# Kernel optimization log

Measured on AMD Instinct MI355X. Metric: run time of the kernel, lower is better.

## Reference

```python
import jax, jax.numpy as jnp
import numpy as np

V, D, H, L, E = 50000, 512, 512, 4, 40000


def setup_inputs() -> dict:
    key = jax.random.key(0)
    k1, k2, k3 = jax.random.split(key, 3)
    node_embeddings = jax.random.normal(k1, (V, D), dtype=jnp.float32)
    adjacency = jax.random.randint(k2, (L, E, 2), 0, V, dtype=jnp.int32)
    W = jax.random.normal(k3, (L, D, H), dtype=jnp.float32) * (1.0 / np.sqrt(D))
    return {"node_embeddings": node_embeddings, "adjacency": adjacency, "W": W}


def reference(node_embeddings, adjacency, W):
    # adjacency: [L, E, 2] with [:, :, 0] = source node, [:, :, 1] = target node
    src = adjacency[..., 0]  # [L, E]
    tgt = adjacency[..., 1]  # [L, E]
    # Gather source states per edge and apply per-edge-type linear message fn.
    # edge_source_states: [L, E, D]; messages: [L, E, H]
    messages = jnp.einsum("led,ldh->leh", node_embeddings[src], W)
    # Scatter-aggregate (sum) all messages to their target nodes.
    num_nodes = node_embeddings.shape[0]
    aggregated = jax.ops.segment_sum(
        messages.reshape(-1, messages.shape[-1]),  # [L*E, H]
        tgt.reshape(-1),
        num_segments=num_nodes,
    )  # [V, H]
    # message_activation_before_aggregation = False -> activation after aggregation
    return jax.nn.relu(aggregated)
```

## Files before the change

### kernel.cpp

```cpp
#include <hip/hip_runtime.h>
#include <hip/hip_bf16.h>

#define NV 50000
#define VP2 50176
#define ND 512
#define NH 512
#define NL 4
#define NE 40000
#define CAP 16
#define KTOT 2048
#define NKT 32
#define NWG2 392

typedef short bf16x8 __attribute__((ext_vector_type(8)));
typedef float f32x4  __attribute__((ext_vector_type(4)));

__device__ __forceinline__ unsigned short f2bf(float f) {
    unsigned int u = __float_as_uint(f);
    u += 0x7FFFu + ((u >> 16) & 1u);
    return (unsigned short)(u >> 16);
}
__device__ __forceinline__ unsigned pack_bf2(float x, float y) {
    return (unsigned)f2bf(x) | ((unsigned)f2bf(y) << 16);
}

#define GLL16(gp, lp) __builtin_amdgcn_global_load_lds( \
    (const __attribute__((address_space(1))) void*)(gp), \
    (__attribute__((address_space(3))) void*)(lp), 16, 0, 0)

#define SBAR   __builtin_amdgcn_s_barrier()
#define SCHED0 __builtin_amdgcn_sched_barrier(0)
#define PRIO1  __builtin_amdgcn_s_setprio(1)
#define PRIO0  __builtin_amdgcn_s_setprio(0)
#define VMCNT0 asm volatile("s_waitcnt vmcnt(0)" ::: "memory")
#define LGKM0  asm volatile("s_waitcnt lgkmcnt(0)" ::: "memory")

__global__ void wt2_kernel(const float* __restrict__ W, unsigned short* __restrict__ Wt2) {
    int idx = blockIdx.x * 256 + threadIdx.x;
    int l = idx >> 18;
    int r = idx & 262143;
    int k = r >> 9;
    int h = r & 511;
    Wt2[((size_t)h << 11) + (l << 9) + k] = f2bf(W[idx]);
}

__global__ void place_kernel(const int* __restrict__ adj, int* __restrict__ cnt,
                             int* __restrict__ list) {
    int i = blockIdx.x * 256 + threadIdx.x;
    int2 p = ((const int2*)adj)[i];
    int l = i / NE;
    int cell = p.y * NL + l;
    int pos = atomicAdd(&cnt[cell], 1);
    if (pos < CAP) list[cell * CAP + pos] = p.x;
}

__global__ void __launch_bounds__(256)
agg_pull(const float* __restrict__ emb, const int* __restrict__ cnt,
         const int* __restrict__ list, unsigned* __restrict__ agg2) {
    const int wid  = blockIdx.x * 4 + (threadIdx.x >> 6);
    const int lane = threadIdx.x & 63;
    const int t    = wid >> 2;
    const int l    = wid & 3;
    const int cell = wid;
    const size_t dst = (size_t)t * 1024 + l * 256 + lane;

    int n = cnt[cell]; if (n > CAP) n = CAP;
    const int* lst = list + cell * CAP;

    float2 s0 = {0.f,0.f}, s1 = {0.f,0.f}, s2 = {0.f,0.f}, s3 = {0.f,0.f};
    int j = 0;
    for (; j + 2 <= n; j += 2) {
        const float2* p0 = (const float2*)(emb + (size_t)lst[j]     * ND) + lane;
        const float2* p1 = (const float2*)(emb + (size_t)lst[j + 1] * ND) + lane;
        float2 a0 = p0[0], a1 = p0[64], a2 = p0[128], a3 = p0[192];
        float2 b0 = p1[0], b1 = p1[64], b2 = p1[128], b3 = p1[192];
        s0.x += a0.x + b0.x; s0.y += a0.y + b0.y;
        s1.x += a1.x + b1.x; s1.y += a1.y + b1.y;
        s2.x += a2.x + b2.x; s2.y += a2.y + b2.y;
        s3.x += a3.x + b3.x; s3.y += a3.y + b3.y;
    }
    if (j < n) {
        const float2* p0 = (const float2*)(emb + (size_t)lst[j] * ND) + lane;
        float2 a0 = p0[0], a1 = p0[64], a2 = p0[128], a3 = p0[192];
        s0.x += a0.x; s0.y += a0.y;  s1.x += a1.x; s1.y += a1.y;
        s2.x += a2.x; s2.y += a2.y;  s3.x += a3.x; s3.y += a3.y;
    }
    agg2[dst]       = pack_bf2(s0.x, s0.y);
    agg2[dst + 64]  = pack_bf2(s1.x, s1.y);
    agg2[dst + 128] = pack_bf2(s2.x, s2.y);
    agg2[dst + 192] = pack_bf2(s3.x, s3.y);
}

__device__ __forceinline__ void stage_ht(
    int s, int t0, int n0, int wave, int lane,
    const unsigned short* __restrict__ agg2, const unsigned short* __restrict__ Wt2,
    unsigned short* sa0, unsigned short* sa1,
    unsigned short* sb0, unsigned short* sb1) {
    const int tile  = s >> 2, part = s & 3;
    const int lr8   = (part & 1) << 7;
    const int rowin = lane >> 3;
    const int slt   = (lane & 7) ^ rowin;
    const bool isA  = part < 2;
    const unsigned short* gsrc = isA ? agg2 : Wt2;
    const int gr0 = isA ? t0 : n0;
    unsigned short* ldsbase = isA ? ((tile & 1) ? sa1 : sa0)
                                  : ((tile & 1) ? sb1 : sb0);
#pragma unroll
    for (int c = 0; c < 2; ++c) {
        const int lr = lr8 + (wave * 2 + c) * 8;
        const unsigned short* src = gsrc
            + (size_t)(gr0 + lr + rowin) * KTOT + tile * 64 + slt * 8;
        GLL16(src, ldsbase + lr * 64);
    }
}

template<bool STG, bool VMW>
__device__ __forceinline__ void group4(
    int kt, int t0, int n0, int wave, int lane, int wm, int wn,
    const unsigned short* __restrict__ agg2, const unsigned short* __restrict__ Wt2,
    unsigned short* sa0, unsigned short* sa1,
    unsigned short* sb0, unsigned short* sb1,
    f32x4 (&acc)[8][4]) {
    const int laneL = lane & 15, laneH = lane >> 4;
    const int ax = laneL & 7;
    const unsigned short* pa = (kt & 1) ? sa1 : sa0;
    const unsigned short* pb = (kt & 1) ? sb1 : sb0;
    const int s1 = (kt + 1) * 4;
    bf16x8 aF[4][2], bF[4][2];

#pragma unroll
    for (int mi = 0; mi < 4; ++mi)
#pragma unroll
        for (int ks = 0; ks < 2; ++ks) {
            const int row = wm * 128 + mi * 16 + laneL;
            aF[mi][ks] = *(const bf16x8*)(pa + row * 64 + (((ks * 4 + laneH) ^ ax) << 3));
        }
#pragma unroll
    for (int ni = 0; ni < 2; ++ni)
#pragma unroll
        for (int ks = 0; ks < 2; ++ks) {
            const int row = wn * 64 + ni * 16 + laneL;
            bF[ni][ks] = *(const bf16x8*)(pb + row * 64 + (((ks * 4 + laneH) ^ ax) << 3));
        }
    if (STG) {
        stage_ht(s1 + 0, t0, n0, wave, lane, agg2, Wt2, sa0, sa1, sb0, sb1);
        stage_ht(s1 + 1, t0, n0, wave, lane, agg2, Wt2, sa0, sa1, sb0, sb1);
    }
    SBAR; LGKM0; SCHED0; PRIO1;
#pragma unroll
    for (int mi = 0; mi < 4; ++mi)
#pragma unroll
        for (int ni = 0; ni < 2; ++ni)
#pragma unroll
            for (int ks = 0; ks < 2; ++ks)
                acc[mi][ni] = __builtin_amdgcn_mfma_f32_16x16x32_bf16(aF[mi][ks], bF[ni][ks], acc[mi][ni], 0, 0, 0);
    PRIO0; SBAR;

#pragma unroll
    for (int ni = 0; ni < 2; ++ni)
#pragma unroll
        for (int ks = 0; ks < 2; ++ks) {
            const int row = wn * 64 + (ni + 2) * 16 + laneL;
            bF[ni + 2][ks] = *(const bf16x8*)(pb + row * 64 + (((ks * 4 + laneH) ^ ax) << 3));
        }
    if (STG) stage_ht(s1 + 2, t0, n0, wave, lane, agg2, Wt2, sa0, sa1, sb0, sb1);
    SBAR; LGKM0; SCHED0; PRIO1;
#pragma unroll
    for (int mi = 0; mi < 4; ++mi)
#pragma unroll
        for (int ni = 0; ni < 2; ++ni)
#pragma unroll
            for (int ks = 0; ks < 2; ++ks)
                acc[mi][ni + 2] = __builtin_amdgcn_mfma_f32_16x16x32_bf16(aF[mi][ks], bF[ni + 2][ks], acc[mi][ni + 2], 0, 0, 0);
    PRIO0; SBAR;

#pragma unroll
    for (int mi = 0; mi < 4; ++mi)
#pragma unroll
        for (int ks = 0; ks < 2; ++ks) {
            const int row = wm * 128 + (mi + 4) * 16 + laneL;
            aF[mi][ks] = *(const bf16x8*)(pa + row * 64 + (((ks * 4 + laneH) ^ ax) << 3));
        }
    if (STG) stage_ht(s1 + 3, t0, n0, wave, lane, agg2, Wt2, sa0, sa1, sb0, sb1);
    SBAR; LGKM0; SCHED0; PRIO1;
#pragma unroll
    for (int mi = 0; mi < 4; ++mi)
#pragma unroll
        for (int ni = 0; ni < 2; ++ni)
#pragma unroll
            for (int ks = 0; ks < 2; ++ks)
                acc[mi + 4][ni] = __builtin_amdgcn_mfma_f32_16x16x32_bf16(aF[mi][ks], bF[ni][ks], acc[mi + 4][ni], 0, 0, 0);
    PRIO0; SBAR;

    PRIO1;
#pragma unroll
    for (int mi = 0; mi < 4; ++mi)
#pragma unroll
        for (int ni = 0; ni < 2; ++ni)
#pragma unroll
            for (int ks = 0; ks < 2; ++ks)
                acc[mi + 4][ni + 2] = __builtin_amdgcn_mfma_f32_16x16x32_bf16(aF[mi][ks], bF[ni + 2][ks], acc[mi + 4][ni + 2], 0, 0, 0);
    PRIO0;
    if (VMW) { VMCNT0; }
    SBAR;
}

__global__ void __launch_bounds__(512)
gemm8(const unsigned short* __restrict__ agg2,
      const unsigned short* __restrict__ Wt2,
      float* __restrict__ out) {
    __shared__ unsigned short s_a[2][256 * 64];
    __shared__ unsigned short s_b[2][256 * 64];

    const int orig = blockIdx.x;
    const int wgid = (orig & 7) * (NWG2 / 8) + (orig >> 3);
    const int mt = wgid >> 1, nt = wgid & 1;
    const int t0 = mt * 256, n0 = nt * 256;

    const int tid  = threadIdx.x;
    const int lane = tid & 63;
    const int wave = tid >> 6;
    const int wm   = wave >> 2;
    const int wn   = wave & 3;
    const int laneL = lane & 15, laneH = lane >> 4;

    f32x4 acc[8][4];
#pragma unroll
    for (int mi = 0; mi < 8; ++mi)
#pragma unroll
        for (int ni = 0; ni < 4; ++ni)
            acc[mi][ni] = (f32x4){0.f, 0.f, 0.f, 0.f};

    unsigned short* sa0 = &s_a[0][0]; unsigned short* sa1 = &s_a[1][0];
    unsigned short* sb0 = &s_b[0][0]; unsigned short* sb1 = &s_b[1][0];

#pragma unroll
    for (int p = 0; p < 4; ++p)
        stage_ht(p, t0, n0, wave, lane, agg2, Wt2, sa0, sa1, sb0, sb1);
    VMCNT0; SCHED0; SBAR;

    for (int ktp = 0; ktp < 15; ++ktp) {
        group4<true, true>(2 * ktp,     t0, n0, wave, lane, wm, wn, agg2, Wt2, sa0, sa1, sb0, sb1, acc);
        group4<true, true>(2 * ktp + 1, t0, n0, wave, lane, wm, wn, agg2, Wt2, sa0, sa1, sb0, sb1, acc);
    }
    group4<true,  true >(30, t0, n0, wave, lane, wm, wn, agg2, Wt2, sa0, sa1, sb0, sb1, acc);
    group4<false, false>(31, t0, n0, wave, lane, wm, wn, agg2, Wt2, sa0, sa1, sb0, sb1, acc);

#pragma unroll
    for (int mi = 0; mi < 8; ++mi) {
#pragma unroll
        for (int i = 0; i < 4; ++i) {
            int t = t0 + wm * 128 + mi * 16 + laneH * 4 + i;
            if (t < NV) {
#pragma unroll
                for (int ni = 0; ni < 4; ++ni) {
                    int h = n0 + wn * 64 + ni * 16 + laneL;
                    out[(size_t)t * NH + h] = fmaxf(acc[mi][ni][i], 0.f);
                }
            }
        }
    }
}

__global__ void wt_legacy(const float* __restrict__ W, unsigned short* __restrict__ Wt) {
    int idx = blockIdx.x * 256 + threadIdx.x;
    int l = idx >> 18;
    int r = idx & 262143;
    int k = r >> 9;
    int h = r & 511;
    Wt[(l << 18) + (h << 9) + k] = f2bf(W[idx]);
}
__global__ void __launch_bounds__(256)
legacy_msg(const float* __restrict__ emb, const int* __restrict__ adj,
           const unsigned short* __restrict__ Wt, float* __restrict__ out) {
    __shared__ bf16x8 s_a[32 * 64];
    __shared__ int s_src[32];
    __shared__ int s_tgt[32];
    const int bx = blockIdx.x;
    const int l = bx / (NE / 32);
    const int ebase = (bx % (NE / 32)) * 32;
    const int tid = threadIdx.x, lane = tid & 63, wave = tid >> 6;
    if (tid < 32) {
        int2 p = *(const int2*)(adj + ((size_t)l * NE + ebase + tid) * 2);
        s_src[tid] = p.x; s_tgt[tid] = p.y;
    }
    __syncthreads();
    {
        const int r = tid >> 3, part = tid & 7, k0 = part * 64, rxx = r & 7;
        const float* g = emb + (size_t)s_src[r] * ND + k0;
#pragma unroll
        for (int j = 0; j < 8; ++j) {
            float4 f0 = *(const float4*)(g + j * 8);
            float4 f1 = *(const float4*)(g + j * 8 + 4);
            bf16x8 v;
            v[0]=(short)f2bf(f0.x); v[1]=(short)f2bf(f0.y);
            v[2]=(short)f2bf(f0.z); v[3]=(short)f2bf(f0.w);
            v[4]=(short)f2bf(f1.x); v[5]=(short)f2bf(f1.y);
            v[6]=(short)f2bf(f1.z); v[7]=(short)f2bf(f1.w);
            int slot = (k0 >> 3) + j;
            s_a[r * 64 + (slot ^ rxx)] = v;
        }
    }
    __syncthreads();
    const int c0 = wave * 128, laneL = lane & 15, laneH = lane >> 4, arx = laneL & 7;
    f32x4 acc[2][8];
#pragma unroll
    for (int mf = 0; mf < 2; ++mf)
#pragma unroll
        for (int nf = 0; nf < 8; ++nf) acc[mf][nf] = (f32x4){0.f,0.f,0.f,0.f};
    const bf16x8* wb = (const bf16x8*)(Wt + ((size_t)l << 18));
#pragma unroll
    for (int kc = 0; kc < 16; ++kc) {
        int slot = kc * 4 + laneH;
        bf16x8 a0 = s_a[laneL * 64 + (slot ^ arx)];
        bf16x8 a1 = s_a[(16 + laneL) * 64 + (slot ^ arx)];
#pragma unroll
        for (int nf = 0; nf < 8; ++nf) {
            bf16x8 b = wb[(c0 + nf * 16 + laneL) * 64 + slot];
            acc[0][nf] = __builtin_amdgcn_mfma_f32_16x16x32_bf16(a0, b, acc[0][nf], 0, 0, 0);
            acc[1][nf] = __builtin_amdgcn_mfma_f32_16x16x32_bf16(a1, b, acc[1][nf], 0, 0, 0);
        }
    }
#pragma unroll
    for (int mf = 0; mf < 2; ++mf)
#pragma unroll
        for (int nf = 0; nf < 8; ++nf) {
            int h = c0 + nf * 16 + laneL;
#pragma unroll
            for (int i = 0; i < 4; ++i) {
                int er = mf * 16 + laneH * 4 + i;
                atomicAdd(out + (size_t)s_tgt[er] * NH + h, acc[mf][nf][i]);
            }
        }
}
__global__ void legacy_relu(float* __restrict__ o, int n4) {
    int stride = gridDim.x * blockDim.x;
    for (int i = blockIdx.x * blockDim.x + threadIdx.x; i < n4; i += stride) {
        float4 v = ((float4*)o)[i];
        v.x = fmaxf(v.x, 0.f); v.y = fmaxf(v.y, 0.f);
        v.z = fmaxf(v.z, 0.f); v.w = fmaxf(v.w, 0.f);
        ((float4*)o)[i] = v;
    }
}

extern "C" void kernel_launch(void* const* d_in, const int* in_sizes, int n_in,
                              void* d_out, int out_size, void* d_ws, size_t ws_size,
                              hipStream_t stream) {
    const float* emb = (const float*)d_in[0];
    const int*   adj = (const int*)d_in[1];
    const float* W   = (const float*)d_in[2];
    float* out = (float*)d_out;
    char* ws = (char*)d_ws;

    unsigned short* Wt2  = (unsigned short*)ws;
    int*            cnt  = (int*)(ws + 2621440);
    int*            list = (int*)(ws + 3670016);
    unsigned short* agg2 = (unsigned short*)(ws + (16u << 20));

    const size_t need = (16u << 20) + (size_t)VP2 * KTOT * 2;

    if (ws_size >= need) {
        hipMemsetAsync(cnt, 0, (size_t)VP2 * NL * sizeof(int), stream);
        wt2_kernel<<<(NL * ND * NH) / 256, 256, 0, stream>>>(W, Wt2);
        place_kernel<<<(NL * NE) / 256, 256, 0, stream>>>(adj, cnt, list);
        agg_pull<<<(VP2 * NL) / 4, 256, 0, stream>>>(emb, cnt, list, (unsigned*)agg2);
        gemm8<<<NWG2, 512, 0, stream>>>(agg2, Wt2, out);
    } else {
        hipMemsetAsync(d_out, 0, (size_t)out_size * sizeof(float), stream);
        wt_legacy<<<(NL * ND * NH) / 256, 256, 0, stream>>>(W, Wt2);
        legacy_msg<<<NL * (NE / 32), 256, 0, stream>>>(emb, adj, Wt2, out);
        legacy_relu<<<2048, 256, 0, stream>>>(out, out_size / 4);
    }
}
```

Baseline: 272.0 us.

## Replace hand-scheduled pingpong GEMM loop with simple double-buffered tile loop

Replaces the finely interleaved group4 schedule with a plain per-k-tile step. The old schedule split staging across four MFMA sub-blocks, with explicit barriers, priority hints, sched_barrier and waitcnt control. The new step issues all four global-to-LDS stages for the next tile up front, loads all B fragments and then A in two halves, runs the MFMAs, and ends with one __syncthreads. It cuts barrier count and scheduling constraints, but gives up the explicit overlap of LDS reads and MFMAs and relies on the compiler to schedule.

```diff
diff --git a/kernel.cpp b/kernel.cpp
--- a/kernel.cpp
+++ b/kernel.cpp
@@ -27,13 +27,6 @@
 #define GLL16(gp, lp) __builtin_amdgcn_global_load_lds( \
     (const __attribute__((address_space(1))) void*)(gp), \
     (__attribute__((address_space(3))) void*)(lp), 16, 0, 0)
-
-#define SBAR   __builtin_amdgcn_s_barrier()
-#define SCHED0 __builtin_amdgcn_sched_barrier(0)
-#define PRIO1  __builtin_amdgcn_s_setprio(1)
-#define PRIO0  __builtin_amdgcn_s_setprio(0)
-#define VMCNT0 asm volatile("s_waitcnt vmcnt(0)" ::: "memory")
-#define LGKM0  asm volatile("s_waitcnt lgkmcnt(0)" ::: "memory")
 
 __global__ void wt2_kernel(const float* __restrict__ W, unsigned short* __restrict__ Wt2) {
     int idx = blockIdx.x * 256 + threadIdx.x;
@@ -114,8 +107,8 @@
     }
 }
 
-template<bool STG, bool VMW>
-__device__ __forceinline__ void group4(
+template<bool STG>
+__device__ __forceinline__ void tile_step(
     int kt, int t0, int n0, int wave, int lane, int wm, int wn,
     const unsigned short* __restrict__ agg2, const unsigned short* __restrict__ Wt2,
     unsigned short* sa0, unsigned short* sa1,
@@ -125,9 +118,23 @@
     const int ax = laneL & 7;
     const unsigned short* pa = (kt & 1) ? sa1 : sa0;
     const unsigned short* pb = (kt & 1) ? sb1 : sb0;
-    const int s1 = (kt + 1) * 4;
+
+    if (STG) {
+        const int s1 = (kt + 1) * 4;
+        stage_ht(s1 + 0, t0, n0, wave, lane, agg2, Wt2, sa0, sa1, sb0, sb1);
+        stage_ht(s1 + 1, t0, n0, wave, lane, agg2, Wt2, sa0, sa1, sb0, sb1);
+        stage_ht(s1 + 2, t0, n0, wave, lane, agg2, Wt2, sa0, sa1, sb0, sb1);
+        stage_ht(s1 + 3, t0, n0, wave, lane, agg2, Wt2, sa0, sa1, sb0, sb1);
+    }
+
     bf16x8 aF[4][2], bF[4][2];
-
+#pragma unroll
+    for (int ni = 0; ni < 4; ++ni)
+#pragma unroll
+        for (int ks = 0; ks < 2; ++ks) {
+            const int row = wn * 64 + ni * 16 + laneL;
+            bF[ni][ks] = *(const bf16x8*)(pb + row * 64 + (((ks * 4 + laneH) ^ ax) << 3));
+        }
 #pragma unroll
     for (int mi = 0; mi < 4; ++mi)
 #pragma unroll
@@ -136,44 +143,12 @@
             aF[mi][ks] = *(const bf16x8*)(pa + row * 64 + (((ks * 4 + laneH) ^ ax) << 3));
         }
 #pragma unroll
-    for (int ni = 0; ni < 2; ++ni)
-#pragma unroll
-        for (int ks = 0; ks < 2; ++ks) {
-            const int row = wn * 64 + ni * 16 + laneL;
-            bF[ni][ks] = *(const bf16x8*)(pb + row * 64 + (((ks * 4 + laneH) ^ ax) << 3));
-        }
-    if (STG) {
-        stage_ht(s1 + 0, t0, n0, wave, lane, agg2, Wt2, sa0, sa1, sb0, sb1);
-        stage_ht(s1 + 1, t0, n0, wave, lane, agg2, Wt2, sa0, sa1, sb0, sb1);
-    }
-    SBAR; LGKM0; SCHED0; PRIO1;
-#pragma unroll
     for (int mi = 0; mi < 4; ++mi)
 #pragma unroll
-        for (int ni = 0; ni < 2; ++ni)
+        for (int ni = 0; ni < 4; ++ni)
 #pragma unroll
             for (int ks = 0; ks < 2; ++ks)
                 acc[mi][ni] = __builtin_amdgcn_mfma_f32_16x16x32_bf16(aF[mi][ks], bF[ni][ks], acc[mi][ni], 0, 0, 0);
-    PRIO0; SBAR;
-
-#pragma unroll
-    for (int ni = 0; ni < 2; ++ni)
-#pragma unroll
-        for (int ks = 0; ks < 2; ++ks) {
-            const int row = wn * 64 + (ni + 2) * 16 + laneL;
-            bF[ni + 2][ks] = *(const bf16x8*)(pb + row * 64 + (((ks * 4 + laneH) ^ ax) << 3));
-        }
-    if (STG) stage_ht(s1 + 2, t0, n0, wave, lane, agg2, Wt2, sa0, sa1, sb0, sb1);
-    SBAR; LGKM0; SCHED0; PRIO1;
-#pragma unroll
-    for (int mi = 0; mi < 4; ++mi)
-#pragma unroll
-        for (int ni = 0; ni < 2; ++ni)
-#pragma unroll
-            for (int ks = 0; ks < 2; ++ks)
-                acc[mi][ni + 2] = __builtin_amdgcn_mfma_f32_16x16x32_bf16(aF[mi][ks], bF[ni + 2][ks], acc[mi][ni + 2], 0, 0, 0);
-    PRIO0; SBAR;
-
 #pragma unroll
     for (int mi = 0; mi < 4; ++mi)
 #pragma unroll
@@ -181,34 +156,21 @@
             const int row = wm * 128 + (mi + 4) * 16 + laneL;
             aF[mi][ks] = *(const bf16x8*)(pa + row * 64 + (((ks * 4 + laneH) ^ ax) << 3));
         }
-    if (STG) stage_ht(s1 + 3, t0, n0, wave, lane, agg2, Wt2, sa0, sa1, sb0, sb1);
-    SBAR; LGKM0; SCHED0; PRIO1;
 #pragma unroll
     for (int mi = 0; mi < 4; ++mi)
 #pragma unroll
-        for (int ni = 0; ni < 2; ++ni)
+        for (int ni = 0; ni < 4; ++ni)
 #pragma unroll
             for (int ks = 0; ks < 2; ++ks)
                 acc[mi + 4][ni] = __builtin_amdgcn_mfma_f32_16x16x32_bf16(aF[mi][ks], bF[ni][ks], acc[mi + 4][ni], 0, 0, 0);
-    PRIO0; SBAR;
-
-    PRIO1;
-#pragma unroll
-    for (int mi = 0; mi < 4; ++mi)
-#pragma unroll
-        for (int ni = 0; ni < 2; ++ni)
-#pragma unroll
-            for (int ks = 0; ks < 2; ++ks)
-                acc[mi + 4][ni + 2] = __builtin_amdgcn_mfma_f32_16x16x32_bf16(aF[mi][ks], bF[ni + 2][ks], acc[mi + 4][ni + 2], 0, 0, 0);
-    PRIO0;
-    if (VMW) { VMCNT0; }
-    SBAR;
+
+    __syncthreads();
 }
 
 __global__ void __launch_bounds__(512)
-gemm8(const unsigned short* __restrict__ agg2,
-      const unsigned short* __restrict__ Wt2,
-      float* __restrict__ out) {
+gemm2p(const unsigned short* __restrict__ agg2,
+       const unsigned short* __restrict__ Wt2,
+       float* __restrict__ out) {
     __shared__ unsigned short s_a[2][256 * 64];
     __shared__ unsigned short s_b[2][256 * 64];
 
@@ -237,14 +199,11 @@
 #pragma unroll
     for (int p = 0; p < 4; ++p)
         stage_ht(p, t0, n0, wave, lane, agg2, Wt2, sa0, sa1, sb0, sb1);
-    VMCNT0; SCHED0; SBAR;
-
-    for (int ktp = 0; ktp < 15; ++ktp) {
-        group4<true, true>(2 * ktp,     t0, n0, wave, lane, wm, wn, agg2, Wt2, sa0, sa1, sb0, sb1, acc);
-        group4<true, true>(2 * ktp + 1, t0, n0, wave, lane, wm, wn, agg2, Wt2, sa0, sa1, sb0, sb1, acc);
-    }
-    group4<true,  true >(30, t0, n0, wave, lane, wm, wn, agg2, Wt2, sa0, sa1, sb0, sb1, acc);
-    group4<false, false>(31, t0, n0, wave, lane, wm, wn, agg2, Wt2, sa0, sa1, sb0, sb1, acc);
+    __syncthreads();
+
+    for (int kt = 0; kt < NKT - 1; ++kt)
+        tile_step<true>(kt, t0, n0, wave, lane, wm, wn, agg2, Wt2, sa0, sa1, sb0, sb1, acc);
+    tile_step<false>(NKT - 1, t0, n0, wave, lane, wm, wn, agg2, Wt2, sa0, sa1, sb0, sb1, acc);
 
 #pragma unroll
     for (int mi = 0; mi < 8; ++mi) {
@@ -364,7 +323,7 @@
         wt2_kernel<<<(NL * ND * NH) / 256, 256, 0, stream>>>(W, Wt2);
         place_kernel<<<(NL * NE) / 256, 256, 0, stream>>>(adj, cnt, list);
         agg_pull<<<(VP2 * NL) / 4, 256, 0, stream>>>(emb, cnt, list, (unsigned*)agg2);
-        gemm8<<<NWG2, 512, 0, stream>>>(agg2, Wt2, out);
+        gemm2p<<<NWG2, 512, 0, stream>>>(agg2, Wt2, out);
     } else {
         hipMemsetAsync(d_out, 0, (size_t)out_size * sizeof(float), stream);
         wt_legacy<<<(NL * ND * NH) / 256, 256, 0, stream>>>(W, Wt2);
```

Result: faster. 261.2 us, median of 2 (-4.0%).

## Reorder GEMM staging into half-tile chunks with partial vmcnt waits

Applied to the files above, without the earlier changes.

The GEMM main loop now stages one quarter-tile per compute phase and waits with vmcnt(4) instead of vmcnt(0), reordering stage chunks (0,2,3,1). This keeps global-to-LDS loads in flight across phases instead of draining the queue at each group boundary. The wave-to-subtile mapping is also changed so each wave covers interleaved low and high halves of the 256x256 tile, with the epilogue remapped to match. The risk is that the partial-wait ordering could allow reads of LDS data that has not yet arrived if the chunk order is wrong.

```diff
diff --git a/kernel.cpp b/kernel.cpp
--- a/kernel.cpp
+++ b/kernel.cpp
@@ -32,6 +32,7 @@
 #define SCHED0 __builtin_amdgcn_sched_barrier(0)
 #define PRIO1  __builtin_amdgcn_s_setprio(1)
 #define PRIO0  __builtin_amdgcn_s_setprio(0)
+#define VMCNT4 asm volatile("s_waitcnt vmcnt(4)" ::: "memory")
 #define VMCNT0 asm volatile("s_waitcnt vmcnt(0)" ::: "memory")
 #define LGKM0  asm volatile("s_waitcnt lgkmcnt(0)" ::: "memory")
 
@@ -114,8 +115,8 @@
     }
 }
 
-template<bool STG, bool VMW>
-__device__ __forceinline__ void group4(
+template<bool STG, bool LAST>
+__device__ __forceinline__ void tile8(
     int kt, int t0, int n0, int wave, int lane, int wm, int wn,
     const unsigned short* __restrict__ agg2, const unsigned short* __restrict__ Wt2,
     unsigned short* sa0, unsigned short* sa1,
@@ -126,26 +127,23 @@
     const unsigned short* pa = (kt & 1) ? sa1 : sa0;
     const unsigned short* pb = (kt & 1) ? sb1 : sb0;
     const int s1 = (kt + 1) * 4;
-    bf16x8 aF[4][2], bF[4][2];
+    bf16x8 aF[4][2], bLo[2][2], bHi[2][2];
 
 #pragma unroll
     for (int mi = 0; mi < 4; ++mi)
 #pragma unroll
         for (int ks = 0; ks < 2; ++ks) {
-            const int row = wm * 128 + mi * 16 + laneL;
+            const int row = wm * 64 + mi * 16 + laneL;
             aF[mi][ks] = *(const bf16x8*)(pa + row * 64 + (((ks * 4 + laneH) ^ ax) << 3));
         }
 #pragma unroll
     for (int ni = 0; ni < 2; ++ni)
 #pragma unroll
         for (int ks = 0; ks < 2; ++ks) {
-            const int row = wn * 64 + ni * 16 + laneL;
-            bF[ni][ks] = *(const bf16x8*)(pb + row * 64 + (((ks * 4 + laneH) ^ ax) << 3));
-        }
-    if (STG) {
-        stage_ht(s1 + 0, t0, n0, wave, lane, agg2, Wt2, sa0, sa1, sb0, sb1);
-        stage_ht(s1 + 1, t0, n0, wave, lane, agg2, Wt2, sa0, sa1, sb0, sb1);
-    }
+            const int row = wn * 32 + ni * 16 + laneL;
+            bLo[ni][ks] = *(const bf16x8*)(pb + row * 64 + (((ks * 4 + laneH) ^ ax) << 3));
+        }
+    if (STG) stage_ht(s1 + 0, t0, n0, wave, lane, agg2, Wt2, sa0, sa1, sb0, sb1);
     SBAR; LGKM0; SCHED0; PRIO1;
 #pragma unroll
     for (int mi = 0; mi < 4; ++mi)
@@ -153,15 +151,18 @@
         for (int ni = 0; ni < 2; ++ni)
 #pragma unroll
             for (int ks = 0; ks < 2; ++ks)
-                acc[mi][ni] = __builtin_amdgcn_mfma_f32_16x16x32_bf16(aF[mi][ks], bF[ni][ks], acc[mi][ni], 0, 0, 0);
-    PRIO0; SBAR;
+                acc[mi][ni] = __builtin_amdgcn_mfma_f32_16x16x32_bf16(aF[mi][ks], bLo[ni][ks], acc[mi][ni], 0, 0, 0);
+    PRIO0;
+    if (STG) { VMCNT4; SCHED0; }
+    else if (LAST) { VMCNT0; SCHED0; }
+    SBAR;
 
 #pragma unroll
     for (int ni = 0; ni < 2; ++ni)
 #pragma unroll
         for (int ks = 0; ks < 2; ++ks) {
-            const int row = wn * 64 + (ni + 2) * 16 + laneL;
-            bF[ni + 2][ks] = *(const bf16x8*)(pb + row * 64 + (((ks * 4 + laneH) ^ ax) << 3));
+            const int row = 128 + wn * 32 + ni * 16 + laneL;
+            bHi[ni][ks] = *(const bf16x8*)(pb + row * 64 + (((ks * 4 + laneH) ^ ax) << 3));
         }
     if (STG) stage_ht(s1 + 2, t0, n0, wave, lane, agg2, Wt2, sa0, sa1, sb0, sb1);
     SBAR; LGKM0; SCHED0; PRIO1;
@@ -171,14 +172,16 @@
         for (int ni = 0; ni < 2; ++ni)
 #pragma unroll
             for (int ks = 0; ks < 2; ++ks)
-                acc[mi][ni + 2] = __builtin_amdgcn_mfma_f32_16x16x32_bf16(aF[mi][ks], bF[ni + 2][ks], acc[mi][ni + 2], 0, 0, 0);
-    PRIO0; SBAR;
+                acc[mi][ni + 2] = __builtin_amdgcn_mfma_f32_16x16x32_bf16(aF[mi][ks], bHi[ni][ks], acc[mi][ni + 2], 0, 0, 0);
+    PRIO0;
+    if (STG) { VMCNT4; SCHED0; }
+    SBAR;
 
 #pragma unroll
     for (int mi = 0; mi < 4; ++mi)
 #pragma unroll
         for (int ks = 0; ks < 2; ++ks) {
-            const int row = wm * 128 + (mi + 4) * 16 + laneL;
+            const int row = 128 + wm * 64 + mi * 16 + laneL;
             aF[mi][ks] = *(const bf16x8*)(pa + row * 64 + (((ks * 4 + laneH) ^ ax) << 3));
         }
     if (STG) stage_ht(s1 + 3, t0, n0, wave, lane, agg2, Wt2, sa0, sa1, sb0, sb1);
@@ -189,9 +192,10 @@
         for (int ni = 0; ni < 2; ++ni)
 #pragma unroll
             for (int ks = 0; ks < 2; ++ks)
-                acc[mi + 4][ni] = __builtin_amdgcn_mfma_f32_16x16x32_bf16(aF[mi][ks], bF[ni][ks], acc[mi + 4][ni], 0, 0, 0);
+                acc[mi + 4][ni] = __builtin_amdgcn_mfma_f32_16x16x32_bf16(aF[mi][ks], bLo[ni][ks], acc[mi + 4][ni], 0, 0, 0);
     PRIO0; SBAR;
 
+    if (STG) stage_ht(s1 + 1, t0, n0, wave, lane, agg2, Wt2, sa0, sa1, sb0, sb1);
     PRIO1;
 #pragma unroll
     for (int mi = 0; mi < 4; ++mi)
@@ -199,16 +203,16 @@
         for (int ni = 0; ni < 2; ++ni)
 #pragma unroll
             for (int ks = 0; ks < 2; ++ks)
-                acc[mi + 4][ni + 2] = __builtin_amdgcn_mfma_f32_16x16x32_bf16(aF[mi][ks], bF[ni + 2][ks], acc[mi + 4][ni + 2], 0, 0, 0);
+                acc[mi + 4][ni + 2] = __builtin_amdgcn_mfma_f32_16x16x32_bf16(aF[mi][ks], bHi[ni][ks], acc[mi + 4][ni + 2], 0, 0, 0);
     PRIO0;
-    if (VMW) { VMCNT0; }
+    if (STG) { VMCNT4; SCHED0; }
     SBAR;
 }
 
 __global__ void __launch_bounds__(512)
-gemm8(const unsigned short* __restrict__ agg2,
-      const unsigned short* __restrict__ Wt2,
-      float* __restrict__ out) {
+gemm8p(const unsigned short* __restrict__ agg2,
+       const unsigned short* __restrict__ Wt2,
+       float* __restrict__ out) {
     __shared__ unsigned short s_a[2][256 * 64];
     __shared__ unsigned short s_b[2][256 * 64];
 
@@ -234,27 +238,27 @@
     unsigned short* sa0 = &s_a[0][0]; unsigned short* sa1 = &s_a[1][0];
     unsigned short* sb0 = &s_b[0][0]; unsigned short* sb1 = &s_b[1][0];
 
-#pragma unroll
-    for (int p = 0; p < 4; ++p)
-        stage_ht(p, t0, n0, wave, lane, agg2, Wt2, sa0, sa1, sb0, sb1);
-    VMCNT0; SCHED0; SBAR;
-
-    for (int ktp = 0; ktp < 15; ++ktp) {
-        group4<true, true>(2 * ktp,     t0, n0, wave, lane, wm, wn, agg2, Wt2, sa0, sa1, sb0, sb1, acc);
-        group4<true, true>(2 * ktp + 1, t0, n0, wave, lane, wm, wn, agg2, Wt2, sa0, sa1, sb0, sb1, acc);
-    }
-    group4<true,  true >(30, t0, n0, wave, lane, wm, wn, agg2, Wt2, sa0, sa1, sb0, sb1, acc);
-    group4<false, false>(31, t0, n0, wave, lane, wm, wn, agg2, Wt2, sa0, sa1, sb0, sb1, acc);
+    stage_ht(0, t0, n0, wave, lane, agg2, Wt2, sa0, sa1, sb0, sb1);
+    stage_ht(2, t0, n0, wave, lane, agg2, Wt2, sa0, sa1, sb0, sb1);
+    stage_ht(3, t0, n0, wave, lane, agg2, Wt2, sa0, sa1, sb0, sb1);
+    stage_ht(1, t0, n0, wave, lane, agg2, Wt2, sa0, sa1, sb0, sb1);
+    VMCNT4; SCHED0; SBAR;
+
+    for (int kt = 0; kt < NKT - 1; ++kt)
+        tile8<true, false>(kt, t0, n0, wave, lane, wm, wn, agg2, Wt2, sa0, sa1, sb0, sb1, acc);
+    tile8<false, true>(NKT - 1, t0, n0, wave, lane, wm, wn, agg2, Wt2, sa0, sa1, sb0, sb1, acc);
 
 #pragma unroll
     for (int mi = 0; mi < 8; ++mi) {
+        const int rb = (mi < 4) ? (wm * 64 + mi * 16) : (128 + wm * 64 + (mi - 4) * 16);
 #pragma unroll
         for (int i = 0; i < 4; ++i) {
-            int t = t0 + wm * 128 + mi * 16 + laneH * 4 + i;
+            int t = t0 + rb + laneH * 4 + i;
             if (t < NV) {
 #pragma unroll
                 for (int ni = 0; ni < 4; ++ni) {
-                    int h = n0 + wn * 64 + ni * 16 + laneL;
+                    const int cb = (ni < 2) ? (wn * 32 + ni * 16) : (128 + wn * 32 + (ni - 2) * 16);
+                    int h = n0 + cb + laneL;
                     out[(size_t)t * NH + h] = fmaxf(acc[mi][ni][i], 0.f);
                 }
             }
@@ -364,7 +368,7 @@
         wt2_kernel<<<(NL * ND * NH) / 256, 256, 0, stream>>>(W, Wt2);
         place_kernel<<<(NL * NE) / 256, 256, 0, stream>>>(adj, cnt, list);
         agg_pull<<<(VP2 * NL) / 4, 256, 0, stream>>>(emb, cnt, list, (unsigned*)agg2);
-        gemm8<<<NWG2, 512, 0, stream>>>(agg2, Wt2, out);
+        gemm8p<<<NWG2, 512, 0, stream>>>(agg2, Wt2, out);
     } else {
         hipMemsetAsync(d_out, 0, (size_t)out_size * sizeof(float), stream);
         wt_legacy<<<(NL * ND * NH) / 256, 256, 0, stream>>>(W, Wt2);
```

After: 261.8 us. -3.8%, faster.
